# Optimization experiments

Measured on AMD Instinct MI355X. Metric: run time of the kernel, lower is better.

Reference implementation:

```python
import jax, jax.numpy as jnp
import numpy as np

D_MODEL = 1024
NUM_HEADS = 16
HEAD_DIM = D_MODEL // NUM_HEADS


def setup_inputs() -> dict:
    key = jax.random.key(0)
    kx, kq, kk, kv, ko = jax.random.split(key, 5)
    init_std = float(np.sqrt(2.0 / (D_MODEL + D_MODEL)))
    def trunc(k):
        # trunc normal in [-3std, 3std], matching nn.init.trunc_normal_
        return jax.random.truncated_normal(k, -3.0, 3.0, (D_MODEL, D_MODEL), jnp.float32) * init_std
    return {
        "x": jax.random.normal(kx, (2, 2048, D_MODEL), jnp.float32),
        "Wq": trunc(kq),
        "Wk": trunc(kk),
        "Wv": trunc(kv),
        "Wo": trunc(ko),
    }


def reference(x, Wq, Wk, Wv, Wo):
    b, s, _ = x.shape
    # projections: Linear computes x @ W.T with W [out, in]
    q = (x @ Wq.T).reshape(b, s, NUM_HEADS, HEAD_DIM).transpose(0, 2, 1, 3)
    k = (x @ Wk.T).reshape(b, s, NUM_HEADS, HEAD_DIM).transpose(0, 2, 1, 3)
    v = (x @ Wv.T).reshape(b, s, NUM_HEADS, HEAD_DIM).transpose(0, 2, 1, 3)
    scale = 1.0 / jnp.sqrt(jnp.float32(HEAD_DIM))
    logits = jnp.einsum("bhqd,bhkd->bhqk", q, k)  # [b,h,s,s]
    causal = jnp.tril(jnp.ones((s, s), dtype=bool))
    logits = jnp.where(causal, logits, -jnp.inf)
    attn = jax.nn.softmax(logits * scale, axis=-1)
    out = jnp.einsum("bhqk,bhkd->bhqd", attn, v)
    out = out.transpose(0, 2, 1, 3).reshape(b, s, D_MODEL)
    return out @ Wo.T
```

## Files before the change

### kernel.cpp

```cpp
#include <hip/hip_runtime.h>
#include <hip/hip_bf16.h>


#define DEVI __device__ __forceinline__

typedef __bf16 bf16x8 __attribute__((ext_vector_type(8)));
typedef short  short8 __attribute__((ext_vector_type(8)));
typedef float  f32x4  __attribute__((ext_vector_type(4)));
typedef float  f32x16 __attribute__((ext_vector_type(16)));
typedef unsigned int u32x4 __attribute__((ext_vector_type(4)));

DEVI short f2bfs(float f) {
    __hip_bfloat16 h = __float2bfloat16(f);
    return __builtin_bit_cast(short, h);
}
DEVI unsigned pack2rb(float a, float b) {
    const unsigned ua = __builtin_bit_cast(unsigned, a) + 0x8000u;
    const unsigned ub = __builtin_bit_cast(unsigned, b) + 0x8000u;
    return __builtin_amdgcn_perm(ub, ua, 0x07060302u);
}
DEVI bf16x8 ld8(const short* p) {
    return __builtin_bit_cast(bf16x8, *(const short8*)p);
}
DEVI void gload16(const void* g, void* lds) {
    __builtin_amdgcn_global_load_lds(
        (const __attribute__((address_space(1))) void*)g,
        (__attribute__((address_space(3))) void*)lds, 16, 0, 0);
}
DEVI void plswap(unsigned& a, unsigned& b) {
    asm volatile("v_permlane32_swap_b32 %0, %1" : "+v"(a), "+v"(b));
}
DEVI const short* lds_swc(const short* base, int row, int col) {
    return (const short*)((const char*)base + (((row << 7) + (col << 1)) ^ ((row & 7) << 4)));
}

#if defined(__has_builtin)
#if __has_builtin(__builtin_amdgcn_exp2f)
#define HAVE_EXP2 1
#endif
#endif
DEVI float ex2(float x) {
#ifdef HAVE_EXP2
    return __builtin_amdgcn_exp2f(x);
#else
    return __expf(x * 0.69314718055994531f);
#endif
}
#define CEXP 0.18033688011112042f
#define MCF  (64.0f * CEXP)

__global__ __launch_bounds__(256) void convert_kernel(
    const float* __restrict__ x, const float* __restrict__ Wq,
    const float* __restrict__ Wk, const float* __restrict__ Wv,
    const float* __restrict__ Wo, short* __restrict__ xb, short* __restrict__ wb) {
    const int bid = blockIdx.x;
    const float* src;
    short* dst;
    int i8;
    if (bid < 2048) {
        src = x; dst = xb;
        i8 = (bid * 256 + threadIdx.x) * 8;
    } else {
        const int w = bid - 2048;
        const int z = w >> 9;
        src = (z == 0) ? Wq : (z == 1) ? Wk : (z == 2) ? Wv : Wo;
        dst = wb + (size_t)z * 1048576;
        i8 = (((w & 511) * 256) + threadIdx.x) * 8;
    }
    float4 a = ((const float4*)(src + i8))[0];
    float4 b = ((const float4*)(src + i8))[1];
    short8 t;
    t[0] = f2bfs(a.x); t[1] = f2bfs(a.y); t[2] = f2bfs(a.z); t[3] = f2bfs(a.w);
    t[4] = f2bfs(b.x); t[5] = f2bfs(b.y); t[6] = f2bfs(b.z); t[7] = f2bfs(b.w);
    *(short8*)(dst + i8) = t;
}

template <int BM, int BN, int MF, int NF, int WN>
DEVI void gemm_kloop64(const short* __restrict__ A, const short* __restrict__ B,
                       short* As, short* Bs, int wid, int lane, f32x4 acc[MF][NF]) {
    const int l15 = lane & 15, l4 = lane >> 4;
    const int wm = wid / WN, wn = wid % WN;
    const int rowc = lane >> 3;
    const int gcol = ((lane & 7) ^ rowc) * 8;
    constexpr int NCHA = BM / 8, NCHB = BN / 8;
#pragma unroll 1
    for (int k0 = 0; k0 < 1024; k0 += 64) {
        __syncthreads();
#pragma unroll
        for (int c = wid; c < NCHA; c += 4)
            gload16(A + (size_t)(c * 8 + rowc) * 1024 + k0 + gcol, As + c * 512);
#pragma unroll
        for (int c = wid; c < NCHB; c += 4)
            gload16(B + (size_t)(c * 8 + rowc) * 1024 + k0 + gcol, Bs + c * 512);
        __syncthreads();
#pragma unroll
        for (int kk = 0; kk < 2; ++kk) {
            bf16x8 af[MF], bf[NF];
#pragma unroll
            for (int m = 0; m < MF; ++m) {
                const int row = wm * (MF * 16) + m * 16 + l15;
                af[m] = ld8(As + row * 64 + (((kk * 4 + l4) ^ (row & 7)) * 8));
            }
#pragma unroll
            for (int n = 0; n < NF; ++n) {
                const int row = wn * (NF * 16) + n * 16 + l15;
                bf[n] = ld8(Bs + row * 64 + (((kk * 4 + l4) ^ (row & 7)) * 8));
            }
#pragma unroll
            for (int m = 0; m < MF; ++m)
#pragma unroll
                for (int n = 0; n < NF; ++n)
                    acc[m][n] = __builtin_amdgcn_mfma_f32_16x16x32_bf16(af[m], bf[n], acc[m][n], 0, 0, 0);
        }
    }
}

__global__ __launch_bounds__(256) void gemm_qkv_kernel(
    const short* __restrict__ xb, const short* __restrict__ wb,
    short* __restrict__ Qo, short* __restrict__ Ko, short* __restrict__ VtG) {
    __shared__ short As[8192], Bs[8192];
    const int tid = threadIdx.x, lane = tid & 63, wid = tid >> 6;
    const int l15 = lane & 15, l4 = lane >> 4;
    const int wm = wid >> 1, wn = wid & 1;
    const int y = blockIdx.y, wsel = y >> 3;
    const int row0 = blockIdx.x * 128, col0 = (y & 7) * 128;

    f32x4 acc[4][4] = {};
    gemm_kloop64<128, 128, 4, 4, 2>(
        xb + (size_t)row0 * 1024,
        wb + (size_t)wsel * 1048576 + (size_t)col0 * 1024,
        As, Bs, wid, lane, acc);

    if (wsel == 2) {
#pragma unroll
        for (int m = 0; m < 4; ++m)
#pragma unroll
            for (int n = 0; n < 4; ++n)
#pragma unroll
                for (int j = 0; j < 4; ++j) {
                    int row = row0 + wm * 64 + m * 16 + l4 * 4 + j;
                    int col = col0 + wn * 64 + n * 16 + l15;
                    VtG[(size_t)col * 4096 + row] = f2bfs(acc[m][n][j]);
                }
    } else {
        short* C = (wsel == 0) ? Qo : Ko;
#pragma unroll
        for (int m = 0; m < 4; ++m)
#pragma unroll
            for (int n = 0; n < 4; ++n)
#pragma unroll
                for (int j = 0; j < 4; ++j) {
                    int row = row0 + wm * 64 + m * 16 + l4 * 4 + j;
                    int col = col0 + wn * 64 + n * 16 + l15;
                    C[(size_t)row * 1024 + col] = f2bfs(acc[m][n][j]);
                }
    }
}

__global__ __launch_bounds__(256) void gemm_wo_kernel(
    const short* __restrict__ Ao, const short* __restrict__ Wob,
    float* __restrict__ Cout) {
    __shared__ short As[4096], Bs[8192];
    const int tid = threadIdx.x, lane = tid & 63, wid = tid >> 6;
    const int l15 = lane & 15, l4 = lane >> 4;
    const int wn = wid;
    const int row0 = blockIdx.x * 64, col0 = blockIdx.y * 128;

    f32x4 acc[4][2] = {};
    gemm_kloop64<64, 128, 4, 2, 4>(
        Ao + (size_t)row0 * 1024, Wob + (size_t)col0 * 1024,
        As, Bs, wid, lane, acc);

#pragma unroll
    for (int m = 0; m < 4; ++m)
#pragma unroll
        for (int n = 0; n < 2; ++n)
#pragma unroll
            for (int j = 0; j < 4; ++j) {
                const int row = row0 + m * 16 + l4 * 4 + j;
                const int col = col0 + wn * 32 + n * 16 + l15;
                Cout[(size_t)row * 1024 + col] = acc[m][n][j];
            }
}

DEVI void read_frags(const short* Ks, const short* Vts, int l31, int hi,
                     bf16x8 kf[8], bf16x8 vb[8]) {
#pragma unroll
    for (int ds = 0; ds < 4; ++ds) {
        kf[ds]     = ld8(lds_swc(Ks, l31,      ds * 16 + hi * 8));
        kf[4 + ds] = ld8(lds_swc(Ks, 32 + l31, ds * 16 + hi * 8));
    }
#pragma unroll
    for (int c = 0; c < 2; ++c) {
        vb[c * 4 + 0] = ld8(lds_swc(Vts, l31,      c * 32 + hi * 8));
        vb[c * 4 + 1] = ld8(lds_swc(Vts, 32 + l31, c * 32 + hi * 8));
        vb[c * 4 + 2] = ld8(lds_swc(Vts, l31,      c * 32 + 16 + hi * 8));
        vb[c * 4 + 3] = ld8(lds_swc(Vts, 32 + l31, c * 32 + 16 + hi * 8));
    }
}

template <bool DIAG>
DEVI void attn_tile_r(int kv0, const bf16x8 kf[8], const bf16x8 vb[8],
                      const bf16x8 qf[4], f32x16& o0, f32x16& o1,
                      float& l, int qrow, int hi) {
    f32x16 s0 = 0.0f, s1 = 0.0f;
    __builtin_amdgcn_s_setprio(1);
#pragma unroll
    for (int ds = 0; ds < 4; ++ds)
        s0 = __builtin_amdgcn_mfma_f32_32x32x16_bf16(kf[ds], qf[ds], s0, 0, 0, 0);
#pragma unroll
    for (int ds = 0; ds < 4; ++ds)
        s1 = __builtin_amdgcn_mfma_f32_32x32x16_bf16(kf[4 + ds], qf[ds], s1, 0, 0, 0);
    __builtin_amdgcn_s_setprio(0);

    if (DIAG) {
#pragma unroll
        for (int r = 0; r < 16; ++r) {
            const int kvr = kv0 + (r & 3) + 8 * (r >> 2) + 4 * hi;
            if (kvr > qrow)      s0[r] = -3.0e38f;
            if (kvr + 32 > qrow) s1[r] = -3.0e38f;
        }
    }

    float r0 = 0.f, r1 = 0.f, r2 = 0.f, r3 = 0.f;
    unsigned w0[8], w1[8];
#pragma unroll
    for (int i = 0; i < 8; ++i) {
        const float p0 = ex2(__builtin_fmaf(s0[2 * i],     CEXP, -MCF));
        const float p1 = ex2(__builtin_fmaf(s0[2 * i + 1], CEXP, -MCF));
        const float p2 = ex2(__builtin_fmaf(s1[2 * i],     CEXP, -MCF));
        const float p3 = ex2(__builtin_fmaf(s1[2 * i + 1], CEXP, -MCF));
        r0 += p0; r1 += p1; r2 += p2; r3 += p3;
        w0[i] = pack2rb(p0, p1);
        w1[i] = pack2rb(p2, p3);
    }
    l += (r0 + r1) + (r2 + r3);

    __builtin_amdgcn_s_setprio(1);
#pragma unroll
    for (int c = 0; c < 2; ++c) {
        const unsigned* w = (c == 0) ? w0 : w1;
        unsigned a0 = w[0], a2 = w[2]; plswap(a0, a2);
        unsigned a1 = w[1], a3 = w[3]; plswap(a1, a3);
        unsigned a4 = w[4], a6 = w[6]; plswap(a4, a6);
        unsigned a5 = w[5], a7 = w[7]; plswap(a5, a7);
        u32x4 lo, hw;
        lo[0] = a0; lo[1] = a1; lo[2] = a2; lo[3] = a3;
        hw[0] = a4; hw[1] = a5; hw[2] = a6; hw[3] = a7;
        const bf16x8 paL = __builtin_bit_cast(bf16x8, lo);
        const bf16x8 paH = __builtin_bit_cast(bf16x8, hw);

        o0 = __builtin_amdgcn_mfma_f32_32x32x16_bf16(paL, vb[c * 4 + 0], o0, 0, 0, 0);
        o1 = __builtin_amdgcn_mfma_f32_32x32x16_bf16(paL, vb[c * 4 + 1], o1, 0, 0, 0);
        o0 = __builtin_amdgcn_mfma_f32_32x32x16_bf16(paH, vb[c * 4 + 2], o0, 0, 0, 0);
        o1 = __builtin_amdgcn_mfma_f32_32x32x16_bf16(paH, vb[c * 4 + 3], o1, 0, 0, 0);
    }
    __builtin_amdgcn_s_setprio(0);
}

__global__ __launch_bounds__(128) void attn_kernel(
    const short* __restrict__ Q, const short* __restrict__ K,
    const short* __restrict__ VtG, short* __restrict__ O) {
    __shared__ short Kb[4][4096], Vb[4][4096];

    const int tid = threadIdx.x, lane = tid & 63, wid = tid >> 6;
    const int l31 = lane & 31, hi = lane >> 5;
    const int bid = blockIdx.x;
    const int qt = 31 - (bid >> 5);
    const int bh = bid & 31;
    const int b = bh >> 4, h = bh & 15;
    const size_t base = (size_t)b * 2048 * 1024 + (size_t)h * 64;
    const short* Qp = Q + base;
    const short* Kp = K + base;
    const short* Vp = VtG + (size_t)(h * 64) * 4096 + (size_t)b * 2048;
    short* Op = O + base;

    const int q0w = qt * 64 + wid * 32;
    const int qrow = q0w + l31;

    const int srw = lane >> 3;
    const int swc = ((lane & 7) ^ srw) * 8;
    const short* kSrc = Kp + (size_t)srw * 1024 + swc;
    const short* vSrc = Vp + (size_t)srw * 4096 + swc;
    const int cc0 = wid * 4;

    const int nt = qt + 1;

#define ISS(i)                                                                 \
    if ((i) < nt) {                                                            \
        short* Ksb = Kb[(i) & 3];                                              \
        short* Vsb = Vb[(i) & 3];                                              \
        const int kv0i = (i) * 64;                                             \
        _Pragma("unroll")                                                      \
        for (int c = 0; c < 4; ++c) {                                          \
            const int cc = cc0 + c;                                            \
            gload16(kSrc + (size_t)(kv0i + cc * 8) * 1024, Ksb + cc * 512);    \
            gload16(vSrc + (size_t)(cc * 8) * 4096 + kv0i, Vsb + cc * 512);    \
        }                                                                      \
    }

    ISS(0); ISS(1);

    bf16x8 qf[4];
#pragma unroll
    for (int ds = 0; ds < 4; ++ds)
        qf[ds] = ld8(Qp + (size_t)qrow * 1024 + ds * 16 + hi * 8);

    asm volatile("s_waitcnt vmcnt(0)" ::: "memory");
    __builtin_amdgcn_s_barrier();
    __builtin_amdgcn_sched_barrier(0);

    bf16x8 kf0[8], vb0[8], kf1[8], vb1[8];
    read_frags(Kb[0], Vb[0], l31, hi, kf0, vb0);
    if (nt > 1) read_frags(Kb[1], Vb[1], l31, hi, kf1, vb1);
    __builtin_amdgcn_sched_barrier(0);
    ISS(2); ISS(3);

    f32x16 o0 = 0.0f, o1 = 0.0f;
    float l = 0.0f;

    int t = 0;
#pragma unroll 1
    while (t + 1 < nt) {
        attn_tile_r<false>(t * 64, kf0, vb0, qf, o0, o1, l, qrow, hi);
        if (t + 1 == nt - 1)
            attn_tile_r<true>((t + 1) * 64, kf1, vb1, qf, o0, o1, l, qrow, hi);
        else
            attn_tile_r<false>((t + 1) * 64, kf1, vb1, qf, o0, o1, l, qrow, hi);
        t += 2;
        if (t < nt) {
            asm volatile("s_waitcnt lgkmcnt(0) vmcnt(0)" ::: "memory");
            __builtin_amdgcn_s_barrier();
            __builtin_amdgcn_sched_barrier(0);
            read_frags(Kb[t & 3], Vb[t & 3], l31, hi, kf0, vb0);
            if (t + 1 < nt) read_frags(Kb[(t + 1) & 3], Vb[(t + 1) & 3], l31, hi, kf1, vb1);
            __builtin_amdgcn_sched_barrier(0);
            ISS(t + 2); ISS(t + 3);
        }
    }
    if (t < nt)
        attn_tile_r<true>(t * 64, kf0, vb0, qf, o0, o1, l, qrow, hi);
#undef ISS

    const float lt = l + __shfl_xor(l, 32, 64);
    const float il = 1.0f / lt;
#pragma unroll
    for (int r = 0; r < 16; ++r) {
        const int cr = (r & 3) + 8 * (r >> 2) + 4 * hi;
        const float s = __shfl(il, cr, 64);
        const size_t row = (size_t)(q0w + cr) * 1024;
        Op[row + l31]      = f2bfs(o0[r] * s);
        Op[row + 32 + l31] = f2bfs(o1[r] * s);
    }
}

extern "C" void kernel_launch(void* const* d_in, const int* in_sizes, int n_in,
                              void* d_out, int out_size, void* d_ws, size_t ws_size,
                              hipStream_t stream) {
    const float* x  = (const float*)d_in[0];
    const float* Wq = (const float*)d_in[1];
    const float* Wk = (const float*)d_in[2];
    const float* Wv = (const float*)d_in[3];
    const float* Wo = (const float*)d_in[4];

    short* wb  = (short*)d_ws;
    short* Qw  = wb + (size_t)4 * 1048576;
    short* Kw  = Qw + (size_t)4194304;
    short* Vtw = Kw + (size_t)4194304;
    short* xb  = (short*)d_out;

    convert_kernel<<<4096, 256, 0, stream>>>(x, Wq, Wk, Wv, Wo, xb, wb);
    gemm_qkv_kernel<<<dim3(32, 24), 256, 0, stream>>>(xb, wb, Qw, Kw, Vtw);
    attn_kernel<<<1024, 128, 0, stream>>>(Qw, Kw, Vtw, Qw);
    gemm_wo_kernel<<<dim3(64, 8), 256, 0, stream>>>(Qw, wb + (size_t)3 * 1048576, (float*)d_out);
}
```

Before: 107.7 us.

## Halve attention LDS ring to two buffers and remap QKV GEMM blocks per XCD

The attention kernel now uses two K/V LDS buffers instead of a four-deep ring. Each iteration copies fragments into registers, hits a barrier, then issues the next two tiles' loads into the freed buffers while computing. This halves LDS use per block, which may allow more resident blocks, but it shortens the prefetch distance. The QKV GEMM moves to a 1D grid with an XCD-aware block mapping, so blocks sharing a weight column slice land on the same XCD for L2 reuse.

```diff
diff --git a/kernel.cpp b/kernel.cpp
--- a/kernel.cpp
+++ b/kernel.cpp
@@ -122,8 +122,12 @@
     const int tid = threadIdx.x, lane = tid & 63, wid = tid >> 6;
     const int l15 = lane & 15, l4 = lane >> 4;
     const int wm = wid >> 1, wn = wid & 1;
-    const int y = blockIdx.y, wsel = y >> 3;
-    const int row0 = blockIdx.x * 128, col0 = (y & 7) * 128;
+    const int bid = blockIdx.x;
+    const int xcd = bid & 7, idx = bid >> 3;
+    const int y = xcd * 3 + (idx >> 5);
+    const int xtile = idx & 31;
+    const int wsel = y >> 3;
+    const int row0 = xtile * 128, col0 = (y & 7) * 128;
 
     f32x4 acc[4][4] = {};
     gemm_kloop64<128, 128, 4, 4, 2>(
@@ -261,7 +265,7 @@
 __global__ __launch_bounds__(128) void attn_kernel(
     const short* __restrict__ Q, const short* __restrict__ K,
     const short* __restrict__ VtG, short* __restrict__ O) {
-    __shared__ short Kb[4][4096], Vb[4][4096];
+    __shared__ short KbA[4096], VbA[4096], KbB[4096], VbB[4096];
 
     const int tid = threadIdx.x, lane = tid & 63, wid = tid >> 6;
     const int l31 = lane & 31, hi = lane >> 5;
@@ -286,20 +290,18 @@
 
     const int nt = qt + 1;
 
-#define ISS(i)                                                                 \
+#define ISS(i, Ksb, Vsb)                                                       \
     if ((i) < nt) {                                                            \
-        short* Ksb = Kb[(i) & 3];                                              \
-        short* Vsb = Vb[(i) & 3];                                              \
         const int kv0i = (i) * 64;                                             \
         _Pragma("unroll")                                                      \
         for (int c = 0; c < 4; ++c) {                                          \
             const int cc = cc0 + c;                                            \
-            gload16(kSrc + (size_t)(kv0i + cc * 8) * 1024, Ksb + cc * 512);    \
-            gload16(vSrc + (size_t)(cc * 8) * 4096 + kv0i, Vsb + cc * 512);    \
+            gload16(kSrc + (size_t)(kv0i + cc * 8) * 1024, (Ksb) + cc * 512);  \
+            gload16(vSrc + (size_t)(cc * 8) * 4096 + kv0i, (Vsb) + cc * 512);  \
         }                                                                      \
     }
 
-    ISS(0); ISS(1);
+    ISS(0, KbA, VbA); ISS(1, KbB, VbB);
 
     bf16x8 qf[4];
 #pragma unroll
@@ -310,36 +312,38 @@
     __builtin_amdgcn_s_barrier();
     __builtin_amdgcn_sched_barrier(0);
 
-    bf16x8 kf0[8], vb0[8], kf1[8], vb1[8];
-    read_frags(Kb[0], Vb[0], l31, hi, kf0, vb0);
-    if (nt > 1) read_frags(Kb[1], Vb[1], l31, hi, kf1, vb1);
-    __builtin_amdgcn_sched_barrier(0);
-    ISS(2); ISS(3);
-
     f32x16 o0 = 0.0f, o1 = 0.0f;
     float l = 0.0f;
+    bf16x8 kf0[8], vb0[8], kf1[8], vb1[8];
 
     int t = 0;
 #pragma unroll 1
-    while (t + 1 < nt) {
-        attn_tile_r<false>(t * 64, kf0, vb0, qf, o0, o1, l, qrow, hi);
-        if (t + 1 == nt - 1)
-            attn_tile_r<true>((t + 1) * 64, kf1, vb1, qf, o0, o1, l, qrow, hi);
+    while (t < nt) {
+        read_frags(KbA, VbA, l31, hi, kf0, vb0);
+        if (t + 1 < nt) read_frags(KbB, VbB, l31, hi, kf1, vb1);
+        asm volatile("s_waitcnt lgkmcnt(0)" ::: "memory");
+        __builtin_amdgcn_s_barrier();
+        __builtin_amdgcn_sched_barrier(0);
+        ISS(t + 2, KbA, VbA);
+        ISS(t + 3, KbB, VbB);
+        __builtin_amdgcn_sched_barrier(0);
+        if (t == nt - 1)
+            attn_tile_r<true>(t * 64, kf0, vb0, qf, o0, o1, l, qrow, hi);
         else
-            attn_tile_r<false>((t + 1) * 64, kf1, vb1, qf, o0, o1, l, qrow, hi);
+            attn_tile_r<false>(t * 64, kf0, vb0, qf, o0, o1, l, qrow, hi);
+        if (t + 1 < nt) {
+            if (t + 1 == nt - 1)
+                attn_tile_r<true>((t + 1) * 64, kf1, vb1, qf, o0, o1, l, qrow, hi);
+            else
+                attn_tile_r<false>((t + 1) * 64, kf1, vb1, qf, o0, o1, l, qrow, hi);
+        }
         t += 2;
         if (t < nt) {
-            asm volatile("s_waitcnt lgkmcnt(0) vmcnt(0)" ::: "memory");
+            asm volatile("s_waitcnt vmcnt(0)" ::: "memory");
             __builtin_amdgcn_s_barrier();
             __builtin_amdgcn_sched_barrier(0);
-            read_frags(Kb[t & 3], Vb[t & 3], l31, hi, kf0, vb0);
-            if (t + 1 < nt) read_frags(Kb[(t + 1) & 3], Vb[(t + 1) & 3], l31, hi, kf1, vb1);
-            __builtin_amdgcn_sched_barrier(0);
-            ISS(t + 2); ISS(t + 3);
         }
     }
-    if (t < nt)
-        attn_tile_r<true>(t * 64, kf0, vb0, qf, o0, o1, l, qrow, hi);
 #undef ISS
 
     const float lt = l + __shfl_xor(l, 32, 64);
@@ -370,7 +374,7 @@
     short* xb  = (short*)d_out;
 
     convert_kernel<<<4096, 256, 0, stream>>>(x, Wq, Wk, Wv, Wo, xb, wb);
-    gemm_qkv_kernel<<<dim3(32, 24), 256, 0, stream>>>(xb, wb, Qw, Kw, Vtw);
+    gemm_qkv_kernel<<<768, 256, 0, stream>>>(xb, wb, Qw, Kw, Vtw);
     attn_kernel<<<1024, 128, 0, stream>>>(Qw, Kw, Vtw, Qw);
     gemm_wo_kernel<<<dim3(64, 8), 256, 0, stream>>>(Qw, wb + (size_t)3 * 1048576, (float*)d_out);
 }
```

Result: slower. 114.2 us (+6.0%).
